# Kernel optimization log

Hardware: AMD Instinct MI355X
Metric: run time of the kernel (lower is better)

Reference implementation:

```python
import jax, jax.numpy as jnp
import numpy as np

# Spiking-neuron constants (ALIF_Neuron / output_Neuron are not in the given
# source; we use the standard surrogate-gradient spiking update from this repo
# family: mem = prev*decay*(1-spike) + input; spike = Heaviside(mem-thresh)).
THRESH = 0.5
LENS = 0.5
DECAY = 0.2

B, T, I, H = 64, 512, 256, 512

@jax.custom_vjp
def spike_fn(v):
    return (v > THRESH).astype(v.dtype)

def _spike_fwd(v):
    return spike_fn(v), v

def _spike_bwd(v, g):
    sg = (jnp.abs(v - THRESH) < LENS).astype(v.dtype) / (2.0 * LENS)
    return (g * sg,)

spike_fn.defvjp(_spike_fwd, _spike_bwd)


def setup_inputs() -> dict:
    key = jax.random.key(0)
    ks = jax.random.split(key, 7)
    sc = 0.05
    return {
        "x": jax.random.normal(ks[0], (B, T, I), jnp.float32),
        "Wx0": jax.random.normal(ks[1], (I, 4 * H), jnp.float32) * sc,
        "Wh0": jax.random.normal(ks[2], (H, 4 * H), jnp.float32) * sc,
        "bh0": jax.random.normal(ks[3], (4 * H,), jnp.float32) * sc,
        "Wx1": jax.random.normal(ks[4], (H, 4 * H), jnp.float32) * sc,
        "Wh1": jax.random.normal(ks[5], (H, 4 * H), jnp.float32) * sc,
        "bh1": jax.random.normal(ks[6], (4 * H,), jnp.float32) * sc,
    }


def _cell(xt, s, h, c, Wx, Wh, bh, is_output):
    # ifgo: [B, 4H]; chunk order i, f, g, o as in the torch code
    ifgo = xt @ Wx + h @ Wh + bh
    i, f, g, o = jnp.split(ifgo, 4, axis=-1)
    c_next = jax.nn.sigmoid(f) * c + jax.nn.sigmoid(i) * jnp.tanh(g)
    h_next = jax.nn.sigmoid(o) * jnp.tanh(c_next)
    if is_output:
        # output_Neuron(x, h_next): leaky integration of membrane with input
        h_next = h_next * DECAY + xt
        return s, h_next, c_next
    # ALIF_Neuron(s, h_next, s): adaptive mem update + surrogate spike
    mem = s * DECAY * (1.0 - s) + h_next
    s_new = spike_fn(mem)
    return s_new, mem, c_next


def reference(x, Wx0, Wh0, bh0, Wx1, Wh1, bh1):
    Bb = x.shape[0]
    z = jnp.zeros((Bb, H), x.dtype)
    init = (z, z, z, z, z, z)  # s0, h0, c0, s1, h1, c1

    def step(carry, xt):
        s0, h0, c0, s1, h1, c1 = carry
        s0, h0, c0 = _cell(xt, s0, h0, c0, Wx0, Wh0, bh0, False)
        # layer 1 consumes the spike output s0 of layer 0
        s1, h1, c1 = _cell(s0, s1, h1, c1, Wx1, Wh1, bh1, True)
        return (s0, h0, c0, s1, h1, c1), h1

    xs = jnp.swapaxes(x, 0, 1)  # [T, B, I]
    carry, outs = jax.lax.scan(step, init, xs)
    out = jnp.swapaxes(outs, 0, 1)  # [B, T, H] (batch_first)
    s0, h0, c0, s1, h1, c1 = carry
    s = jnp.stack([s0, s1])
    h = jnp.stack([h0, h1])
    c = jnp.stack([c0, c1])
    return out, s, h, c
```

## Files before the change

kernel.cpp:

```cpp
#include <hip/hip_runtime.h>
#include <math.h>

typedef float vf4 __attribute__((ext_vector_type(4)));

constexpr int T  = 512;
constexpr int BB = 64;
constexpr int II = 256;
constexpr int HH = 512;

constexpr int SOFF = BB * T * HH;
constexpr int HOFF = SOFF + 2 * BB * HH;
constexpr int COFF = HOFF + 2 * BB * HH;

constexpr int WS_WC0 = 0;
constexpr int WS_WC1 = 1572864;
constexpr int WS_BH0 = 3670016;
constexpr int WS_BH1 = 3672064;
constexpr int WS_HX0 = 3674112;
constexpr int WS_HX1 = 3739648;
constexpr int WS_FLG = 3809280;

__device__ __forceinline__ void bypass_st(float* p, float v) {
  asm volatile("global_store_dword %0, %1, off sc1" :: "v"(p), "v"(v) : "memory");
}
__device__ __forceinline__ void bypass_st_u32(unsigned* p, unsigned v) {
  asm volatile("global_store_dword %0, %1, off sc1" :: "v"(p), "v"(v) : "memory");
}
__device__ __forceinline__ unsigned bypass_ldu(const unsigned* p) {
  unsigned r;
  asm volatile("global_load_dword %0, %1, off sc1\n\ts_waitcnt vmcnt(0)"
               : "=&v"(r) : "v"(p) : "memory");
  return r;
}
__device__ __forceinline__ void bypass_ld2x4(const vf4* p0, const vf4* p1, vf4& r0, vf4& r1) {
  asm volatile(
      "global_load_dwordx4 %0, %2, off sc1\n\t"
      "global_load_dwordx4 %1, %3, off sc1\n\t"
      "s_waitcnt vmcnt(0)"
      : "=&v"(r0), "=&v"(r1) : "v"(p0), "v"(p1) : "memory");
}
__device__ __forceinline__ void release_drain() {
  asm volatile("s_waitcnt vmcnt(0)" ::: "memory");
}

__device__ __forceinline__ float sigf(float x) { return 1.0f / (1.0f + __expf(-x)); }
__device__ __forceinline__ float tanh_fast(float x) {
  return 1.0f - 2.0f / (1.0f + __expf(2.0f * x));
}

__device__ __forceinline__ float sxor(float v, int m) { return __shfl_xor(v, m, 64); }
__device__ __forceinline__ vf4 sxor4(vf4 v, int m) {
  vf4 r; r.x = sxor(v.x, m); r.y = sxor(v.y, m); r.z = sxor(v.z, m); r.w = sxor(v.w, m);
  return r;
}

__device__ __forceinline__ int rev3(int v) {
  return ((v & 1) << 2) | (v & 2) | ((v >> 2) & 1);
}

__device__ __forceinline__ vf4 reduce8(const vf4* acc, int kl) {
  const int sel = kl & 1;
  vf4 n0[4];
#pragma unroll
  for (int i = 0; i < 4; ++i) {
    vf4 snd = sel ? acc[i] : acc[i + 4];
    vf4 kp  = sel ? acc[i + 4] : acc[i];
    n0[i] = kp + sxor4(snd, 1);
  }
  const int sel2 = (kl >> 1) & 1;
  vf4 n1[2];
#pragma unroll
  for (int i = 0; i < 2; ++i) {
    vf4 snd = sel2 ? n0[i] : n0[i + 2];
    vf4 kp  = sel2 ? n0[i + 2] : n0[i];
    n1[i] = kp + sxor4(snd, 2);
  }
  const int sel3 = (kl >> 2) & 1;
  vf4 snd = sel3 ? n1[0] : n1[1];
  vf4 kp  = sel3 ? n1[1] : n1[0];
  vf4 r = kp + sxor4(snd, 4);
  r += sxor4(r, 8);
  r += sxor4(r, 16);
  r += sxor4(r, 32);
  return r;
}

__global__ void pack_wc(const float* __restrict__ A, const float* __restrict__ B,
                        int Ka, int K, float* __restrict__ Wp) {
  const int j = blockIdx.x;
  for (int k = threadIdx.x; k < K; k += 256) {
    const float* src = (k < Ka) ? (A + (size_t)k * 2048) : (B + (size_t)(k - Ka) * 2048);
    vf4 v = {src[j], src[512 + j], src[1024 + j], src[1536 + j]};
    ((vf4*)Wp)[(size_t)j * K + k] = v;
  }
}

__global__ void pack_bias(const float* __restrict__ bh0, const float* __restrict__ bh1,
                          float* __restrict__ bh0p, float* __restrict__ bh1p) {
  const int i = blockIdx.x * blockDim.x + threadIdx.x;
  if (i < 2048) {
    bh0p[i] = bh0[(i & 3) * 512 + (i >> 2)];
  } else {
    int q = i - 2048;
    bh1p[q] = bh1[(q & 3) * 512 + (q >> 2)];
  }
}

__global__ __launch_bounds__(1024, 1) void aslstm_main(
    const vf4* __restrict__ Wc0p, const vf4* __restrict__ Wc1p,
    const vf4* __restrict__ bh0p, const vf4* __restrict__ bh1p,
    const float* __restrict__ x,
    float* __restrict__ hx0, float* __restrict__ hx1,
    unsigned* __restrict__ flags,
    float* __restrict__ out) {
  const int wg  = blockIdx.x;
  const int xcd = wg & 7;
  const int a   = wg >> 3;
  const int g   = a & 7;
  const int s   = (a >> 3) * 8 + xcd;
  const int tid = threadIdx.x;
  const int jo  = tid >> 6;
  const int kl  = tid & 63;
  const int j   = s * 16 + jo;
  const int b_loc  = rev3(kl & 7);
  const int b_glob = g * 8 + b_loc;
  const bool rep0  = (kl < 8);

  __shared__ float cat0[8][776];
  __shared__ float cat1[8][1032];

  float c0 = 0.0f, c1 = 0.0f, sp = 0.0f;

  const int pl = (jo << 1) | (kl >> 5);
  const int lc = kl & 31;
  const int js = pl * 16 + (lc >> 1);
  const int b0 = (lc & 1) * 4;
  const int fo = g * 4096 + pl * 128 + lc * 4;
  const bool poller = ((kl & 31) == 0);

  if (tid < 512) {
    int bx = tid >> 6, kx = (tid & 63) * 4;
    *(vf4*)&cat0[bx][kx] = *(const vf4*)&x[(size_t)(g * 8 + bx) * (T * II) + kx];
  }
  {
    int bz = tid >> 7, kz = (tid & 127) * 4;
    *(vf4*)&cat0[bz][256 + kz] = vf4{0.0f, 0.0f, 0.0f, 0.0f};
  }
  __syncthreads();

  for (int t = 0; t < T; ++t) {
    vf4 acc[8];
#pragma unroll
    for (int b = 0; b < 8; ++b) acc[b] = vf4{0, 0, 0, 0};
    {
      const vf4* wr = Wc0p + (size_t)j * 768;
#pragma unroll
      for (int ig = 0; ig < 3; ++ig) {
        const int k0 = ig * 256 + kl * 4;
        vf4 w0 = wr[k0], w1 = wr[k0 + 1], w2 = wr[k0 + 2], w3 = wr[k0 + 3];
#pragma unroll
        for (int b = 0; b < 8; ++b) {
          vf4 av = *(const vf4*)&cat0[b][k0];
          acc[b] += av.x * w0; acc[b] += av.y * w1;
          acc[b] += av.z * w2; acc[b] += av.w * w3;
        }
      }
    }

    {
      vf4 p = reduce8(acc, kl) + bh0p[j];
      float cn  = sigf(p.y) * c0 + sigf(p.x) * tanh_fast(p.z);
      float mem = sigf(p.w) * tanh_fast(cn);
      float sn  = (mem > 0.5f) ? 1.0f : 0.0f;
      c0 = cn; sp = sn;
      if (rep0) {
        bypass_st(&hx0[(t & 1) * 32768 + g * 4096 + j * 8 + b_loc], mem);
        if (t == T - 1) {
          out[SOFF + b_glob * 512 + j] = sn;
          out[HOFF + b_glob * 512 + j] = mem;
          out[COFF + b_glob * 512 + j] = cn;
        }
      }
    }

    vf4 xv = vf4{0, 0, 0, 0};
    if (tid < 512 && t < T - 1) {
      int bx = tid >> 6, kx = (tid & 63) * 4;
      xv = *(const vf4*)&x[(size_t)(g * 8 + bx) * (T * II) + (size_t)(t + 1) * II + kx];
    }

    release_drain();
    __syncthreads();
    if (tid == 0) bypass_st_u32(&flags[g * 64 + s], (unsigned)(t + 1));

    {
      const unsigned tgt = (unsigned)(t + 1);
      const unsigned* fp = &flags[g * 64 + pl];
      for (;;) {
        unsigned v = tgt;
        if (poller) v = bypass_ldu(fp);
        if (__all((int)(v >= tgt))) break;
        __builtin_amdgcn_s_sleep(1);
      }
      const vf4* mp = (const vf4*)(hx0 + (t & 1) * 32768 + fo);
      const vf4* hp = (const vf4*)(hx1 + ((t + 1) & 1) * 32768 + fo);
      vf4 mv, hv;
      bypass_ld2x4(mp, hp, mv, hv);
      cat0[b0 + 0][256 + js] = mv.x;
      cat0[b0 + 1][256 + js] = mv.y;
      cat0[b0 + 2][256 + js] = mv.z;
      cat0[b0 + 3][256 + js] = mv.w;
      cat1[b0 + 0][js] = (mv.x > 0.5f) ? 1.0f : 0.0f;
      cat1[b0 + 1][js] = (mv.y > 0.5f) ? 1.0f : 0.0f;
      cat1[b0 + 2][js] = (mv.z > 0.5f) ? 1.0f : 0.0f;
      cat1[b0 + 3][js] = (mv.w > 0.5f) ? 1.0f : 0.0f;
      cat1[b0 + 0][512 + js] = hv.x;
      cat1[b0 + 1][512 + js] = hv.y;
      cat1[b0 + 2][512 + js] = hv.z;
      cat1[b0 + 3][512 + js] = hv.w;
      if (tid < 512) {
        int bx = tid >> 6, kx = (tid & 63) * 4;
        *(vf4*)&cat0[bx][kx] = xv;
      }
    }
    __syncthreads();

#pragma unroll
    for (int b = 0; b < 8; ++b) acc[b] = vf4{0, 0, 0, 0};
    {
      const vf4* wr = Wc1p + (size_t)j * 1024;
#pragma unroll
      for (int ig = 0; ig < 4; ++ig) {
        const int k0 = ig * 256 + kl * 4;
        vf4 w0 = wr[k0], w1 = wr[k0 + 1], w2 = wr[k0 + 2], w3 = wr[k0 + 3];
#pragma unroll
        for (int b = 0; b < 8; ++b) {
          vf4 av = *(const vf4*)&cat1[b][k0];
          acc[b] += av.x * w0; acc[b] += av.y * w1;
          acc[b] += av.z * w2; acc[b] += av.w * w3;
        }
      }
    }

    {
      vf4 p = reduce8(acc, kl) + bh1p[j];
      float cn  = sigf(p.y) * c1 + sigf(p.x) * tanh_fast(p.z);
      float hn  = sigf(p.w) * tanh_fast(cn);
      float h1n = hn * 0.2f + sp;
      c1 = cn;
      if (rep0) {
        bypass_st(&hx1[(t & 1) * 32768 + g * 4096 + j * 8 + b_loc], h1n);
        out[(size_t)b_glob * (T * HH) + (size_t)t * HH + j] = h1n;
        if (t == T - 1) {
          out[HOFF + 32768 + b_glob * 512 + j] = h1n;
          out[COFF + 32768 + b_glob * 512 + j] = cn;
        }
      }
    }
  }
}

extern "C" void kernel_launch(void* const* d_in, const int* in_sizes, int n_in,
                              void* d_out, int out_size, void* d_ws, size_t ws_size,
                              hipStream_t stream) {
  const float* x   = (const float*)d_in[0];
  const float* Wx0 = (const float*)d_in[1];
  const float* Wh0 = (const float*)d_in[2];
  const float* bh0 = (const float*)d_in[3];
  const float* Wx1 = (const float*)d_in[4];
  const float* Wh1 = (const float*)d_in[5];
  const float* bh1 = (const float*)d_in[6];
  float* out = (float*)d_out;
  float* ws  = (float*)d_ws;

  float* Wc0p  = ws + WS_WC0;
  float* Wc1p  = ws + WS_WC1;
  float* bh0pf = ws + WS_BH0;
  float* bh1pf = ws + WS_BH1;
  float* hx0   = ws + WS_HX0;
  float* hx1   = ws + WS_HX1;
  unsigned* flags = (unsigned*)(ws + WS_FLG);

  hipMemsetAsync(hx0, 0, 2 * 64 * 512 * sizeof(float), stream);
  hipMemsetAsync(hx1, 0, 2 * 64 * 512 * sizeof(float), stream);
  hipMemsetAsync(flags, 0, 512 * sizeof(unsigned), stream);
  hipMemsetAsync(out + SOFF + BB * HH, 0, BB * HH * sizeof(float), stream);

  pack_wc<<<dim3(512), dim3(256), 0, stream>>>(Wx0, Wh0, 256, 768, Wc0p);
  pack_wc<<<dim3(512), dim3(256), 0, stream>>>(Wx1, Wh1, 512, 1024, Wc1p);
  pack_bias<<<dim3(16), dim3(256), 0, stream>>>(bh0, bh1, bh0pf, bh1pf);

  aslstm_main<<<dim3(256), dim3(1024), 0, stream>>>(
      (const vf4*)Wc0p, (const vf4*)Wc1p, (const vf4*)bh0pf, (const vf4*)bh1pf,
      x, hx0, hx1, flags, out);
}
```

Measured before the change: 7.855 ms.

## Replace flag-based grid barrier with value-tagged data polling and double-buffered LDS

Drops the per-workgroup flag store/poll and the pre-flag __syncthreads/drain. Each published hidden value now carries an offset (+4 or +8, alternating every two steps) that marks which step wrote it, and consumers spin directly on the data loads until every tag matches. The LDS staging buffers are double-buffered so one __syncthreads per step is enough. This removes a round trip and a barrier from the per-step critical path. The cost is that correctness depends on values staying inside the tag windows (mem in (-2,2)), and the offset add and subtract can lose a little float precision.

```diff
diff --git a/kernel.cpp b/kernel.cpp
--- a/kernel.cpp
+++ b/kernel.cpp
@@ -18,19 +18,9 @@
 constexpr int WS_BH1 = 3672064;
 constexpr int WS_HX0 = 3674112;
 constexpr int WS_HX1 = 3739648;
-constexpr int WS_FLG = 3809280;
 
 __device__ __forceinline__ void bypass_st(float* p, float v) {
   asm volatile("global_store_dword %0, %1, off sc1" :: "v"(p), "v"(v) : "memory");
-}
-__device__ __forceinline__ void bypass_st_u32(unsigned* p, unsigned v) {
-  asm volatile("global_store_dword %0, %1, off sc1" :: "v"(p), "v"(v) : "memory");
-}
-__device__ __forceinline__ unsigned bypass_ldu(const unsigned* p) {
-  unsigned r;
-  asm volatile("global_load_dword %0, %1, off sc1\n\ts_waitcnt vmcnt(0)"
-               : "=&v"(r) : "v"(p) : "memory");
-  return r;
 }
 __device__ __forceinline__ void bypass_ld2x4(const vf4* p0, const vf4* p1, vf4& r0, vf4& r1) {
   asm volatile(
@@ -39,8 +29,9 @@
       "s_waitcnt vmcnt(0)"
       : "=&v"(r0), "=&v"(r1) : "v"(p0), "v"(p1) : "memory");
 }
-__device__ __forceinline__ void release_drain() {
-  asm volatile("s_waitcnt vmcnt(0)" ::: "memory");
+
+__device__ __forceinline__ bool tag_ok(float v, bool hi) {
+  return hi ? (v > 6.0f) : (v > 2.0f && v < 6.0f);
 }
 
 __device__ __forceinline__ float sigf(float x) { return 1.0f / (1.0f + __expf(-x)); }
@@ -106,12 +97,15 @@
   }
 }
 
+__global__ void fill_tag(float* __restrict__ p, float v) {
+  p[blockIdx.x * 1024 + threadIdx.x] = v;
+}
+
 __global__ __launch_bounds__(1024, 1) void aslstm_main(
     const vf4* __restrict__ Wc0p, const vf4* __restrict__ Wc1p,
     const vf4* __restrict__ bh0p, const vf4* __restrict__ bh1p,
     const float* __restrict__ x,
     float* __restrict__ hx0, float* __restrict__ hx1,
-    unsigned* __restrict__ flags,
     float* __restrict__ out) {
   const int wg  = blockIdx.x;
   const int xcd = wg & 7;
@@ -126,8 +120,8 @@
   const int b_glob = g * 8 + b_loc;
   const bool rep0  = (kl < 8);
 
-  __shared__ float cat0[8][776];
-  __shared__ float cat1[8][1032];
+  __shared__ float cat0[2][8][776];
+  __shared__ float cat1[2][8][1032];
 
   float c0 = 0.0f, c1 = 0.0f, sp = 0.0f;
 
@@ -136,19 +130,24 @@
   const int js = pl * 16 + (lc >> 1);
   const int b0 = (lc & 1) * 4;
   const int fo = g * 4096 + pl * 128 + lc * 4;
-  const bool poller = ((kl & 31) == 0);
 
   if (tid < 512) {
     int bx = tid >> 6, kx = (tid & 63) * 4;
-    *(vf4*)&cat0[bx][kx] = *(const vf4*)&x[(size_t)(g * 8 + bx) * (T * II) + kx];
+    *(vf4*)&cat0[0][bx][kx] = *(const vf4*)&x[(size_t)(g * 8 + bx) * (T * II) + kx];
   }
   {
     int bz = tid >> 7, kz = (tid & 127) * 4;
-    *(vf4*)&cat0[bz][256 + kz] = vf4{0.0f, 0.0f, 0.0f, 0.0f};
+    *(vf4*)&cat0[0][bz][256 + kz] = vf4{0.0f, 0.0f, 0.0f, 0.0f};
   }
   __syncthreads();
 
   for (int t = 0; t < T; ++t) {
+    const int p0 = t & 1, p1 = p0 ^ 1;
+    const bool tagm = ((t >> 1) & 1) != 0;
+    const bool tagh = (((t + 3) >> 1) & 1) != 0;
+    const float offm = tagm ? 8.0f : 4.0f;
+    const float offh = tagh ? 8.0f : 4.0f;
+
     vf4 acc[8];
 #pragma unroll
     for (int b = 0; b < 8; ++b) acc[b] = vf4{0, 0, 0, 0};
@@ -160,7 +159,7 @@
         vf4 w0 = wr[k0], w1 = wr[k0 + 1], w2 = wr[k0 + 2], w3 = wr[k0 + 3];
 #pragma unroll
         for (int b = 0; b < 8; ++b) {
-          vf4 av = *(const vf4*)&cat0[b][k0];
+          vf4 av = *(const vf4*)&cat0[p0][b][k0];
           acc[b] += av.x * w0; acc[b] += av.y * w1;
           acc[b] += av.z * w2; acc[b] += av.w * w3;
         }
@@ -174,7 +173,7 @@
       float sn  = (mem > 0.5f) ? 1.0f : 0.0f;
       c0 = cn; sp = sn;
       if (rep0) {
-        bypass_st(&hx0[(t & 1) * 32768 + g * 4096 + j * 8 + b_loc], mem);
+        bypass_st(&hx0[p0 * 32768 + g * 4096 + j * 8 + b_loc], mem + offm);
         if (t == T - 1) {
           out[SOFF + b_glob * 512 + j] = sn;
           out[HOFF + b_glob * 512 + j] = mem;
@@ -189,38 +188,37 @@
       xv = *(const vf4*)&x[(size_t)(g * 8 + bx) * (T * II) + (size_t)(t + 1) * II + kx];
     }
 
-    release_drain();
-    __syncthreads();
-    if (tid == 0) bypass_st_u32(&flags[g * 64 + s], (unsigned)(t + 1));
-
-    {
-      const unsigned tgt = (unsigned)(t + 1);
-      const unsigned* fp = &flags[g * 64 + pl];
+    {
+      const vf4* mp = (const vf4*)(hx0 + p0 * 32768 + fo);
+      const vf4* hp = (const vf4*)(hx1 + p1 * 32768 + fo);
+      vf4 mv, hv;
       for (;;) {
-        unsigned v = tgt;
-        if (poller) v = bypass_ldu(fp);
-        if (__all((int)(v >= tgt))) break;
-        __builtin_amdgcn_s_sleep(1);
-      }
-      const vf4* mp = (const vf4*)(hx0 + (t & 1) * 32768 + fo);
-      const vf4* hp = (const vf4*)(hx1 + ((t + 1) & 1) * 32768 + fo);
-      vf4 mv, hv;
-      bypass_ld2x4(mp, hp, mv, hv);
-      cat0[b0 + 0][256 + js] = mv.x;
-      cat0[b0 + 1][256 + js] = mv.y;
-      cat0[b0 + 2][256 + js] = mv.z;
-      cat0[b0 + 3][256 + js] = mv.w;
-      cat1[b0 + 0][js] = (mv.x > 0.5f) ? 1.0f : 0.0f;
-      cat1[b0 + 1][js] = (mv.y > 0.5f) ? 1.0f : 0.0f;
-      cat1[b0 + 2][js] = (mv.z > 0.5f) ? 1.0f : 0.0f;
-      cat1[b0 + 3][js] = (mv.w > 0.5f) ? 1.0f : 0.0f;
-      cat1[b0 + 0][512 + js] = hv.x;
-      cat1[b0 + 1][512 + js] = hv.y;
-      cat1[b0 + 2][512 + js] = hv.z;
-      cat1[b0 + 3][512 + js] = hv.w;
+        bypass_ld2x4(mp, hp, mv, hv);
+        bool ok = tag_ok(mv.x, tagm) && tag_ok(mv.y, tagm) &&
+                  tag_ok(mv.z, tagm) && tag_ok(mv.w, tagm) &&
+                  tag_ok(hv.x, tagh) && tag_ok(hv.y, tagh) &&
+                  tag_ok(hv.z, tagh) && tag_ok(hv.w, tagh);
+        if (__all(ok)) break;
+      }
+      const vf4 om = {offm, offm, offm, offm};
+      const vf4 oh = {offh, offh, offh, offh};
+      vf4 mm = mv - om;
+      vf4 hh = hv - oh;
+      cat0[p1][b0 + 0][256 + js] = mm.x;
+      cat0[p1][b0 + 1][256 + js] = mm.y;
+      cat0[p1][b0 + 2][256 + js] = mm.z;
+      cat0[p1][b0 + 3][256 + js] = mm.w;
+      cat1[p0][b0 + 0][js] = (mm.x > 0.5f) ? 1.0f : 0.0f;
+      cat1[p0][b0 + 1][js] = (mm.y > 0.5f) ? 1.0f : 0.0f;
+      cat1[p0][b0 + 2][js] = (mm.z > 0.5f) ? 1.0f : 0.0f;
+      cat1[p0][b0 + 3][js] = (mm.w > 0.5f) ? 1.0f : 0.0f;
+      cat1[p0][b0 + 0][512 + js] = hh.x;
+      cat1[p0][b0 + 1][512 + js] = hh.y;
+      cat1[p0][b0 + 2][512 + js] = hh.z;
+      cat1[p0][b0 + 3][512 + js] = hh.w;
       if (tid < 512) {
         int bx = tid >> 6, kx = (tid & 63) * 4;
-        *(vf4*)&cat0[bx][kx] = xv;
+        *(vf4*)&cat0[p1][bx][kx] = xv;
       }
     }
     __syncthreads();
@@ -235,7 +233,7 @@
         vf4 w0 = wr[k0], w1 = wr[k0 + 1], w2 = wr[k0 + 2], w3 = wr[k0 + 3];
 #pragma unroll
         for (int b = 0; b < 8; ++b) {
-          vf4 av = *(const vf4*)&cat1[b][k0];
+          vf4 av = *(const vf4*)&cat1[p0][b][k0];
           acc[b] += av.x * w0; acc[b] += av.y * w1;
           acc[b] += av.z * w2; acc[b] += av.w * w3;
         }
@@ -249,7 +247,7 @@
       float h1n = hn * 0.2f + sp;
       c1 = cn;
       if (rep0) {
-        bypass_st(&hx1[(t & 1) * 32768 + g * 4096 + j * 8 + b_loc], h1n);
+        bypass_st(&hx1[p0 * 32768 + g * 4096 + j * 8 + b_loc], h1n + offm);
         out[(size_t)b_glob * (T * HH) + (size_t)t * HH + j] = h1n;
         if (t == T - 1) {
           out[HOFF + 32768 + b_glob * 512 + j] = h1n;
@@ -279,18 +277,17 @@
   float* bh1pf = ws + WS_BH1;
   float* hx0   = ws + WS_HX0;
   float* hx1   = ws + WS_HX1;
-  unsigned* flags = (unsigned*)(ws + WS_FLG);
 
   hipMemsetAsync(hx0, 0, 2 * 64 * 512 * sizeof(float), stream);
-  hipMemsetAsync(hx1, 0, 2 * 64 * 512 * sizeof(float), stream);
-  hipMemsetAsync(flags, 0, 512 * sizeof(unsigned), stream);
+  hipMemsetAsync(hx1, 0, 64 * 512 * sizeof(float), stream);
   hipMemsetAsync(out + SOFF + BB * HH, 0, BB * HH * sizeof(float), stream);
 
   pack_wc<<<dim3(512), dim3(256), 0, stream>>>(Wx0, Wh0, 256, 768, Wc0p);
   pack_wc<<<dim3(512), dim3(256), 0, stream>>>(Wx1, Wh1, 512, 1024, Wc1p);
   pack_bias<<<dim3(16), dim3(256), 0, stream>>>(bh0, bh1, bh0pf, bh1pf);
+  fill_tag<<<dim3(32), dim3(1024), 0, stream>>>(hx1 + 32768, 8.0f);
 
   aslstm_main<<<dim3(256), dim3(1024), 0, stream>>>(
       (const vf4*)Wc0p, (const vf4*)Wc1p, (const vf4*)bh0pf, (const vf4*)bh1pf,
-      x, hx0, hx1, flags, out);
-}
+      x, hx0, hx1, out);
+}
```

Result: faster. 7.677 ms (-2.3%).
